# Kernel tuning notes

Hardware: AMD Instinct MI355X
Metric: run time of the kernel (lower is better)

Reference implementation:

```python
import jax, jax.numpy as jnp
import numpy as np


def _maxpool2(t):
    # 2x2x2 max pool, stride 2. t: [B, C, D, H, W]
    B, C, D, H, W = t.shape
    return t.reshape(B, C, D // 2, 2, H // 2, 2, W // 2, 2).max(axis=(3, 5, 7))


def setup_inputs() -> dict:
    key = jax.random.key(0)
    ks = jax.random.split(key, 5)
    ch = 64
    B, D, H, W = 2, 32, 32, 32
    x = jax.random.normal(ks[0], (B, ch, D, H, W), dtype=jnp.float32)
    # 1x1x1 conv weights (out_ch, in_ch), Kaiming-ish scale
    w_theta = jax.random.normal(ks[1], (ch // 8, ch), dtype=jnp.float32) / np.sqrt(ch)
    w_phi = jax.random.normal(ks[2], (ch // 8, ch), dtype=jnp.float32) / np.sqrt(ch)
    w_g = jax.random.normal(ks[3], (ch // 2, ch), dtype=jnp.float32) / np.sqrt(ch)
    w_o = jax.random.normal(ks[4], (ch, ch // 2), dtype=jnp.float32) / np.sqrt(ch // 2)
    gamma = jnp.ones((), dtype=jnp.float32)  # original inits at 0; 1 gives nontrivial output
    return {"x": x, "w_theta": w_theta, "w_phi": w_phi, "w_g": w_g, "w_o": w_o, "gamma": gamma}


def reference(x, w_theta, w_phi, w_g, w_o, gamma):
    B, C, D, H, W = x.shape
    N = D * H * W
    M = N // 8
    xf = x.reshape(B, C, N)  # [B, C, N]
    # 1x1x1 convs = channel matmuls
    theta = jnp.einsum('oc,bcn->bon', w_theta, xf)                     # [B, C//8, N]
    phi = _maxpool2(jnp.einsum('oc,bcn->bon', w_phi, xf).reshape(B, C // 8, D, H, W)).reshape(B, C // 8, M)
    g = _maxpool2(jnp.einsum('oc,bcn->bon', w_g, xf).reshape(B, C // 2, D, H, W)).reshape(B, C // 2, M)
    # unscaled attention: softmax over keys (M)
    beta = jax.nn.softmax(jnp.einsum('bcn,bcm->bnm', theta, phi), axis=-1)  # [B, N, M]
    o = jnp.einsum('bcm,bnm->bcn', g, beta)                                 # [B, C//2, N]
    out = gamma * jnp.einsum('oc,bcn->bon', w_o, o).reshape(B, C, D, H, W) + x
    return out
```

## Files before the change

### kernel.cpp

```cpp
#include <hip/hip_runtime.h>
#include <cstdint>
#include <cstddef>

typedef __attribute__((ext_vector_type(4))) short short4v;
typedef __attribute__((ext_vector_type(4))) float float4v;

#define C_IN  64
#define NB    2
#define NPTS  32768
#define MPTS  4096
#define LOG2E 1.44269504088896340736f
#define KT    64
#define NTILE (MPTS / KT)
#define QTILES (NPTS / 32)

__device__ __forceinline__ unsigned short f2bf_rne(float f) {
  unsigned int u = __builtin_bit_cast(unsigned int, f);
  u += 0x7fffu + ((u >> 16) & 1u);
  return (unsigned short)(u >> 16);
}

__device__ __forceinline__ short4v pack_bf16_trunc(float a0, float a1, float a2, float a3) {
  unsigned int u0 = __builtin_amdgcn_perm(__builtin_bit_cast(unsigned int, a1),
                                          __builtin_bit_cast(unsigned int, a0), 0x07060302u);
  unsigned int u1 = __builtin_amdgcn_perm(__builtin_bit_cast(unsigned int, a3),
                                          __builtin_bit_cast(unsigned int, a2), 0x07060302u);
  union { unsigned int u[2]; short4v s; } r;
  r.u[0] = u0; r.u[1] = u1;
  return r.s;
}

__device__ __forceinline__ short4v pack_bf16_rne(float a0, float a1, float a2, float a3) {
  short4v s;
  s[0] = (short)f2bf_rne(a0); s[1] = (short)f2bf_rne(a1);
  s[2] = (short)f2bf_rne(a2); s[3] = (short)f2bf_rne(a3);
  return s;
}

__device__ __forceinline__ void gl_lds16(const unsigned short* g, unsigned short* l) {
  __builtin_amdgcn_global_load_lds(
      (const __attribute__((address_space(1))) void*)g,
      (__attribute__((address_space(3))) void*)l, 16, 0, 0);
}


__device__ void pool_body(int idx, const float* __restrict__ x,
                          const float* __restrict__ w_phi,
                          const float* __restrict__ w_g,
                          unsigned short* __restrict__ phi_f,
                          unsigned short* __restrict__ g_f) {
  int cg = idx >> 13;
  int bm = idx & 8191;
  int b = bm >> 12, m = bm & 4095;
  int md = m >> 8, mh = (m >> 4) & 15, mw = m & 15;
  const float* xb = x + (size_t)b * C_IN * NPTS
                  + ((md * 2) * 1024 + (mh * 2) * 32 + (mw * 2));
  const float* wbase = (cg == 0) ? w_phi : (w_g + (cg - 1) * 8 * C_IN);

  float acc[8][8];
#pragma unroll
  for (int o = 0; o < 8; ++o)
#pragma unroll
    for (int p = 0; p < 8; ++p) acc[o][p] = 0.f;

#pragma unroll 4
  for (int cc = 0; cc < C_IN; ++cc) {
    const float* xp = xb + (size_t)cc * NPTS;
    float2 p01 = *(const float2*)(xp + 0);
    float2 p23 = *(const float2*)(xp + 32);
    float2 p45 = *(const float2*)(xp + 1024);
    float2 p67 = *(const float2*)(xp + 1056);
#pragma unroll
    for (int o = 0; o < 8; ++o) {
      float wv = wbase[o * C_IN + cc];
      acc[o][0] = fmaf(wv, p01.x, acc[o][0]);
      acc[o][1] = fmaf(wv, p01.y, acc[o][1]);
      acc[o][2] = fmaf(wv, p23.x, acc[o][2]);
      acc[o][3] = fmaf(wv, p23.y, acc[o][3]);
      acc[o][4] = fmaf(wv, p45.x, acc[o][4]);
      acc[o][5] = fmaf(wv, p45.y, acc[o][5]);
      acc[o][6] = fmaf(wv, p67.x, acc[o][6]);
      acc[o][7] = fmaf(wv, p67.y, acc[o][7]);
    }
  }
  float mx[8];
#pragma unroll
  for (int o = 0; o < 8; ++o) {
    mx[o] = fmaxf(fmaxf(fmaxf(acc[o][0], acc[o][1]), fmaxf(acc[o][2], acc[o][3])),
                  fmaxf(fmaxf(acc[o][4], acc[o][5]), fmaxf(acc[o][6], acc[o][7])));
  }
  int kt16 = m >> 4, kr = m & 15;
  if (cg == 0) {
    size_t fb = ((size_t)b * 256 + kt16) * 256;
#pragma unroll
    for (int g2 = 0; g2 < 2; ++g2) {
      unsigned int u0 = (unsigned int)f2bf_rne(mx[g2 * 4 + 0] * LOG2E)
                      | ((unsigned int)f2bf_rne(mx[g2 * 4 + 1] * LOG2E) << 16);
      unsigned int u1 = (unsigned int)f2bf_rne(mx[g2 * 4 + 2] * LOG2E)
                      | ((unsigned int)f2bf_rne(mx[g2 * 4 + 3] * LOG2E) << 16);
      *(uint2*)&phi_f[fb + (g2 * 16 + kr) * 4] = make_uint2(u0, u1);
    }
#pragma unroll
    for (int g2 = 2; g2 < 4; ++g2) {
      *(uint2*)&phi_f[fb + (g2 * 16 + kr) * 4] = make_uint2(0u, 0u);
    }
  } else {
    int gc0 = (cg - 1) * 8;
#pragma unroll
    for (int o = 0; o < 8; ++o) {
      int c = gc0 + o;
      int half = c >> 4, c15 = c & 15;
      size_t base = (((size_t)b * 256 + kt16) * 2 + half) * 256;
      g_f[base + ((kr >> 2) * 16 + c15) * 4 + (kr & 3)] = f2bf_rne(mx[o]);
    }
  }
}

__device__ void theta_body(int idx, const float* __restrict__ x,
                           const float* __restrict__ w_theta,
                           unsigned short* __restrict__ theta_pad) {
  int b = idx >> 15, n = idx & 32767;
  const float* xb = x + (size_t)b * C_IN * NPTS + n;
  float t[8];
#pragma unroll
  for (int o = 0; o < 8; ++o) t[o] = 0.f;
#pragma unroll 4
  for (int cc = 0; cc < C_IN; ++cc) {
    float xv = xb[(size_t)cc * NPTS];
#pragma unroll
    for (int o = 0; o < 8; ++o) t[o] = fmaf(w_theta[o * C_IN + cc], xv, t[o]);
  }
  unsigned int w0 = (unsigned int)f2bf_rne(t[0]) | ((unsigned int)f2bf_rne(t[1]) << 16);
  unsigned int w1 = (unsigned int)f2bf_rne(t[2]) | ((unsigned int)f2bf_rne(t[3]) << 16);
  unsigned int w2 = (unsigned int)f2bf_rne(t[4]) | ((unsigned int)f2bf_rne(t[5]) << 16);
  unsigned int w3 = (unsigned int)f2bf_rne(t[6]) | ((unsigned int)f2bf_rne(t[7]) << 16);
  uint4* dst = (uint4*)(theta_pad + ((size_t)idx << 4));
  dst[0] = make_uint4(w0, w1, w2, w3);
  dst[1] = make_uint4(0u, 0u, 0u, 0u);
}

__global__ __launch_bounds__(256) void prep_fused(
    const float* __restrict__ x, const float* __restrict__ w_theta,
    const float* __restrict__ w_phi, const float* __restrict__ w_g,
    unsigned short* __restrict__ theta_pad,
    unsigned short* __restrict__ phi_f,
    unsigned short* __restrict__ g_f) {
  int gb = blockIdx.x;
  if (gb < 160) {
    pool_body(gb * 256 + threadIdx.x, x, w_phi, w_g, phi_f, g_f);
  } else {
    theta_body((gb - 160) * 256 + threadIdx.x, x, w_theta, theta_pad);
  }
}

template <int KS>
__global__ __launch_bounds__(256) void attn_split(
    const unsigned short* __restrict__ theta_pad,
    const unsigned short* __restrict__ phi_f,
    const unsigned short* __restrict__ g_f,
    float4v* __restrict__ opart,
    float* __restrict__ lbuf) {
  __shared__ unsigned short s_phi[2][KT * 16];
  __shared__ unsigned short s_g[2][(KT / 16) * 512];

  int tid = threadIdx.x;
  int wid = tid >> 6, lane = tid & 63;
  int l4 = lane >> 4, col = lane & 15;
  int b = blockIdx.y / KS;
  int ks = blockIdx.y & (KS - 1);
  int qb = blockIdx.x * 128 + wid * 32;
  int t0 = ks * (NTILE / KS);
  int t1 = t0 + NTILE / KS;

  const unsigned short* tb = theta_pad + ((size_t)(b * NPTS + qb) << 4) + l4 * 4;
  short4v bt0 = *(const short4v*)(tb + (col << 4));
  short4v bt1 = *(const short4v*)(tb + ((16 + col) << 4));

  const unsigned short* phib = phi_f + (size_t)b * 256 * 256;
  const unsigned short* gb   = g_f + (size_t)b * 256 * 512;

  float4v acc00 = {0.f, 0.f, 0.f, 0.f}, acc01 = acc00, acc10 = acc00, acc11 = acc00;
  float lsum0 = 0.f, lsum1 = 0.f;

  gl_lds16(gb + (size_t)t0 * 2048 + wid * 512 + lane * 8, &s_g[0][wid * 512]);
  if (wid < 2)
    gl_lds16(phib + (size_t)t0 * 1024 + wid * 512 + lane * 8, &s_phi[0][wid * 512]);
  __syncthreads();

#pragma unroll 1
  for (int t = t0; t < t1; ++t) {
    int cur = t & 1;
    if (t + 1 < t1) {
      gl_lds16(gb + (size_t)(t + 1) * 2048 + wid * 512 + lane * 8,
               &s_g[cur ^ 1][wid * 512]);
      if (wid < 2)
        gl_lds16(phib + (size_t)(t + 1) * 1024 + wid * 512 + lane * 8,
                 &s_phi[cur ^ 1][wid * 512]);
    }

#pragma unroll
    for (int st = 0; st < 4; ++st) {
      short4v pf = *(const short4v*)&s_phi[cur][st * 256 + lane * 4];
      short4v g0 = *(const short4v*)&s_g[cur][st * 512 + lane * 4];
      short4v g1 = *(const short4v*)&s_g[cur][st * 512 + 256 + lane * 4];

      float4v zero4 = {0.f, 0.f, 0.f, 0.f};
      float4v s0 = __builtin_amdgcn_mfma_f32_16x16x16bf16_1k(pf, bt0, zero4, 0, 0, 0);
      float4v s1 = __builtin_amdgcn_mfma_f32_16x16x16bf16_1k(pf, bt1, zero4, 0, 0, 0);

      float p00 = __builtin_amdgcn_exp2f(s0[0]);
      float p01 = __builtin_amdgcn_exp2f(s0[1]);
      float p02 = __builtin_amdgcn_exp2f(s0[2]);
      float p03 = __builtin_amdgcn_exp2f(s0[3]);
      float p10 = __builtin_amdgcn_exp2f(s1[0]);
      float p11 = __builtin_amdgcn_exp2f(s1[1]);
      float p12 = __builtin_amdgcn_exp2f(s1[2]);
      float p13 = __builtin_amdgcn_exp2f(s1[3]);
      lsum0 += (p00 + p01) + (p02 + p03);
      lsum1 += (p10 + p11) + (p12 + p13);
      short4v pb0 = pack_bf16_trunc(p00, p01, p02, p03);
      short4v pb1 = pack_bf16_trunc(p10, p11, p12, p13);

      acc00 = __builtin_amdgcn_mfma_f32_16x16x16bf16_1k(g0, pb0, acc00, 0, 0, 0);
      acc01 = __builtin_amdgcn_mfma_f32_16x16x16bf16_1k(g0, pb1, acc01, 0, 0, 0);
      acc10 = __builtin_amdgcn_mfma_f32_16x16x16bf16_1k(g1, pb0, acc10, 0, 0, 0);
      acc11 = __builtin_amdgcn_mfma_f32_16x16x16bf16_1k(g1, pb1, acc11, 0, 0, 0);
    }
    __syncthreads();
  }

  lsum0 += __shfl_xor(lsum0, 16, 64);
  lsum0 += __shfl_xor(lsum0, 32, 64);
  lsum1 += __shfl_xor(lsum1, 16, 64);
  lsum1 += __shfl_xor(lsum1, 32, 64);

  int qt = blockIdx.x * 4 + wid;
  size_t obase = (((size_t)(b * KS + ks) * QTILES + qt) * 4) * 64 + lane;
  opart[obase + 0 * 64] = acc00;
  opart[obase + 1 * 64] = acc01;
  opart[obase + 2 * 64] = acc10;
  opart[obase + 3 * 64] = acc11;
  if (lane < 32) {
    lbuf[((size_t)(b * KS + ks) * QTILES + qt) * 32 + lane] =
        (lane < 16) ? lsum0 : lsum1;
  }
}

template <int KS>
__global__ __launch_bounds__(256) void attn_combine(
    const float* __restrict__ x, const float* __restrict__ w_o,
    const float* __restrict__ gamma_p,
    const float4v* __restrict__ opart,
    const float* __restrict__ lbuf,
    float* __restrict__ out) {
  int tid = threadIdx.x;
  int wid = tid >> 6, lane = tid & 63;
  int l4 = lane >> 4, col = lane & 15;
  int b = blockIdx.y;
  int qt = blockIdx.x * 4 + wid;
  int qb = qt * 32;

  float gamma = gamma_p[0];

  short4v wo[4][2];
#pragma unroll
  for (int cot = 0; cot < 4; ++cot)
#pragma unroll
    for (int ksw = 0; ksw < 2; ++ksw) {
      const float* wp = w_o + (cot * 16 + col) * 32 + ksw * 16 + l4 * 4;
      wo[cot][ksw] = pack_bf16_rne(wp[0] * gamma, wp[1] * gamma,
                                   wp[2] * gamma, wp[3] * gamma);
    }

  float4v a0 = {0.f, 0.f, 0.f, 0.f}, a1 = a0, a2 = a0, a3 = a0;
  float ls0 = 0.f, ls1 = 0.f;
#pragma unroll
  for (int ks = 0; ks < KS; ++ks) {
    size_t ob = (((size_t)(b * KS + ks) * QTILES + qt) * 4) * 64 + lane;
    a0 += opart[ob + 0 * 64];
    a1 += opart[ob + 1 * 64];
    a2 += opart[ob + 2 * 64];
    a3 += opart[ob + 3 * 64];
    const float* lb = lbuf + ((size_t)(b * KS + ks) * QTILES + qt) * 32;
    ls0 += lb[col];
    ls1 += lb[col + 16];
  }
  float li0 = 1.0f / ls0;
  float li1 = 1.0f / ls1;

  short4v onb00 = pack_bf16_rne(a0[0] * li0, a0[1] * li0, a0[2] * li0, a0[3] * li0);
  short4v onb01 = pack_bf16_rne(a1[0] * li1, a1[1] * li1, a1[2] * li1, a1[3] * li1);
  short4v onb10 = pack_bf16_rne(a2[0] * li0, a2[1] * li0, a2[2] * li0, a2[3] * li0);
  short4v onb11 = pack_bf16_rne(a3[0] * li1, a3[1] * li1, a3[2] * li1, a3[3] * li1);

  float4v zero4 = {0.f, 0.f, 0.f, 0.f};
#pragma unroll
  for (int cot = 0; cot < 4; ++cot) {
#pragma unroll
    for (int nt = 0; nt < 2; ++nt) {
      short4v bfrag0 = nt ? onb01 : onb00;
      short4v bfrag1 = nt ? onb11 : onb10;
      float4v d = __builtin_amdgcn_mfma_f32_16x16x16bf16_1k(wo[cot][0], bfrag0, zero4, 0, 0, 0);
      d = __builtin_amdgcn_mfma_f32_16x16x16bf16_1k(wo[cot][1], bfrag1, d, 0, 0, 0);
      int n = qb + nt * 16 + col;
      size_t base = (size_t)(b * C_IN + cot * 16 + l4 * 4) * NPTS + n;
      const float* xp = x + base;
      float* op = out + base;
#pragma unroll
      for (int e = 0; e < 4; ++e) {
        op[(size_t)e * NPTS] = d[e] + xp[(size_t)e * NPTS];
      }
    }
  }
}

__global__ __launch_bounds__(256) void attn_mfma(
    const float* __restrict__ x, const float* __restrict__ w_o,
    const float* __restrict__ gamma_p,
    const unsigned short* __restrict__ theta_pad,
    const unsigned short* __restrict__ phi_f,
    const unsigned short* __restrict__ g_f,
    float* __restrict__ out) {
  __shared__ unsigned short s_phi[2][KT * 16];
  __shared__ unsigned short s_g[2][(KT / 16) * 512];

  int tid = threadIdx.x;
  int wid = tid >> 6, lane = tid & 63;
  int l4 = lane >> 4, col = lane & 15;
  int b = blockIdx.y;
  int qb = blockIdx.x * 128 + wid * 32;

  float gamma = gamma_p[0];

  const unsigned short* tb = theta_pad + ((size_t)(b * NPTS + qb) << 4) + l4 * 4;
  short4v bt0 = *(const short4v*)(tb + (col << 4));
  short4v bt1 = *(const short4v*)(tb + ((16 + col) << 4));

  short4v wo[4][2];
#pragma unroll
  for (int cot = 0; cot < 4; ++cot)
#pragma unroll
    for (int ksw = 0; ksw < 2; ++ksw) {
      const float* wp = w_o + (cot * 16 + col) * 32 + ksw * 16 + l4 * 4;
      wo[cot][ksw] = pack_bf16_rne(wp[0] * gamma, wp[1] * gamma,
                                   wp[2] * gamma, wp[3] * gamma);
    }

  const unsigned short* phib = phi_f + (size_t)b * 256 * 256;
  const unsigned short* gb   = g_f + (size_t)b * 256 * 512;

  float4v acc00 = {0.f, 0.f, 0.f, 0.f}, acc01 = acc00, acc10 = acc00, acc11 = acc00;
  float lsum0 = 0.f, lsum1 = 0.f;

  gl_lds16(gb + 0 * 2048 + wid * 512 + lane * 8, &s_g[0][wid * 512]);
  if (wid < 2)
    gl_lds16(phib + 0 * 1024 + wid * 512 + lane * 8, &s_phi[0][wid * 512]);
  __syncthreads();

#pragma unroll 1
  for (int t = 0; t < NTILE; ++t) {
    int cur = t & 1;
    if (t + 1 < NTILE) {
      gl_lds16(gb + (size_t)(t + 1) * 2048 + wid * 512 + lane * 8,
               &s_g[cur ^ 1][wid * 512]);
      if (wid < 2)
        gl_lds16(phib + (size_t)(t + 1) * 1024 + wid * 512 + lane * 8,
                 &s_phi[cur ^ 1][wid * 512]);
    }
#pragma unroll
    for (int st = 0; st < 4; ++st) {
      short4v pf = *(const short4v*)&s_phi[cur][st * 256 + lane * 4];
      short4v g0 = *(const short4v*)&s_g[cur][st * 512 + lane * 4];
      short4v g1 = *(const short4v*)&s_g[cur][st * 512 + 256 + lane * 4];

      float4v zero4 = {0.f, 0.f, 0.f, 0.f};
      float4v s0 = __builtin_amdgcn_mfma_f32_16x16x16bf16_1k(pf, bt0, zero4, 0, 0, 0);
      float4v s1 = __builtin_amdgcn_mfma_f32_16x16x16bf16_1k(pf, bt1, zero4, 0, 0, 0);

      float p00 = __builtin_amdgcn_exp2f(s0[0]);
      float p01 = __builtin_amdgcn_exp2f(s0[1]);
      float p02 = __builtin_amdgcn_exp2f(s0[2]);
      float p03 = __builtin_amdgcn_exp2f(s0[3]);
      float p10 = __builtin_amdgcn_exp2f(s1[0]);
      float p11 = __builtin_amdgcn_exp2f(s1[1]);
      float p12 = __builtin_amdgcn_exp2f(s1[2]);
      float p13 = __builtin_amdgcn_exp2f(s1[3]);
      lsum0 += (p00 + p01) + (p02 + p03);
      lsum1 += (p10 + p11) + (p12 + p13);
      short4v pb0 = pack_bf16_trunc(p00, p01, p02, p03);
      short4v pb1 = pack_bf16_trunc(p10, p11, p12, p13);

      acc00 = __builtin_amdgcn_mfma_f32_16x16x16bf16_1k(g0, pb0, acc00, 0, 0, 0);
      acc01 = __builtin_amdgcn_mfma_f32_16x16x16bf16_1k(g0, pb1, acc01, 0, 0, 0);
      acc10 = __builtin_amdgcn_mfma_f32_16x16x16bf16_1k(g1, pb0, acc10, 0, 0, 0);
      acc11 = __builtin_amdgcn_mfma_f32_16x16x16bf16_1k(g1, pb1, acc11, 0, 0, 0);
    }
    __syncthreads();
  }

  lsum0 += __shfl_xor(lsum0, 16, 64);
  lsum0 += __shfl_xor(lsum0, 32, 64);
  lsum1 += __shfl_xor(lsum1, 16, 64);
  lsum1 += __shfl_xor(lsum1, 32, 64);
  float li0 = 1.0f / lsum0;
  float li1 = 1.0f / lsum1;

  short4v onb00 = pack_bf16_rne(acc00[0] * li0, acc00[1] * li0, acc00[2] * li0, acc00[3] * li0);
  short4v onb01 = pack_bf16_rne(acc01[0] * li1, acc01[1] * li1, acc01[2] * li1, acc01[3] * li1);
  short4v onb10 = pack_bf16_rne(acc10[0] * li0, acc10[1] * li0, acc10[2] * li0, acc10[3] * li0);
  short4v onb11 = pack_bf16_rne(acc11[0] * li1, acc11[1] * li1, acc11[2] * li1, acc11[3] * li1);

  float4v zero4 = {0.f, 0.f, 0.f, 0.f};
#pragma unroll
  for (int cot = 0; cot < 4; ++cot) {
#pragma unroll
    for (int nt = 0; nt < 2; ++nt) {
      short4v bfrag0 = nt ? onb01 : onb00;
      short4v bfrag1 = nt ? onb11 : onb10;
      float4v d = __builtin_amdgcn_mfma_f32_16x16x16bf16_1k(wo[cot][0], bfrag0, zero4, 0, 0, 0);
      d = __builtin_amdgcn_mfma_f32_16x16x16bf16_1k(wo[cot][1], bfrag1, d, 0, 0, 0);
      int n = qb + nt * 16 + col;
      size_t base = (size_t)(b * C_IN + cot * 16 + l4 * 4) * NPTS + n;
      const float* xp = x + base;
      float* op = out + base;
#pragma unroll
      for (int e = 0; e < 4; ++e) {
        op[(size_t)e * NPTS] = d[e] + xp[(size_t)e * NPTS];
      }
    }
  }
}

extern "C" void kernel_launch(void* const* d_in, const int* in_sizes, int n_in,
                              void* d_out, int out_size, void* d_ws, size_t ws_size,
                              hipStream_t stream) {
  const float* x       = (const float*)d_in[0];
  const float* w_theta = (const float*)d_in[1];
  const float* w_phi   = (const float*)d_in[2];
  const float* w_g     = (const float*)d_in[3];
  const float* w_o     = (const float*)d_in[4];
  const float* gamma   = (const float*)d_in[5];
  float* out = (float*)d_out;

  char* ws = (char*)d_ws;
  unsigned short* theta_pad = (unsigned short*)ws;  ws += (size_t)NB * NPTS * 16 * 2;
  unsigned short* phi_f     = (unsigned short*)ws;  ws += (size_t)NB * 256 * 256 * 2;
  unsigned short* g_f       = (unsigned short*)ws;  ws += (size_t)NB * 256 * 512 * 2;
  size_t base_need = (size_t)(ws - (char*)d_ws);
  float4v* opart = (float4v*)ws;
  size_t opart4 = (size_t)NB * 4 * QTILES * 4 * 64 * sizeof(float4v);
  size_t opart2 = (size_t)NB * 2 * QTILES * 4 * 64 * sizeof(float4v);
  size_t lbuf4  = (size_t)NB * 4 * QTILES * 32 * sizeof(float);
  size_t lbuf2  = (size_t)NB * 2 * QTILES * 32 * sizeof(float);
  size_t need4 = base_need + opart4 + lbuf4;
  size_t need2 = base_need + opart2 + lbuf2;

  prep_fused<<<dim3(416), dim3(256), 0, stream>>>(
      x, w_theta, w_phi, w_g, theta_pad, phi_f, g_f);

  if (ws_size >= need4) {
    float* lbuf = (float*)((char*)opart + opart4);
    attn_split<4><<<dim3(NPTS / 128, NB * 4), dim3(256), 0, stream>>>(
        theta_pad, phi_f, g_f, opart, lbuf);
    attn_combine<4><<<dim3(NPTS / 128, NB), dim3(256), 0, stream>>>(
        x, w_o, gamma, opart, lbuf, out);
  } else if (ws_size >= need2) {
    float* lbuf = (float*)((char*)opart + opart2);
    attn_split<2><<<dim3(NPTS / 128, NB * 2), dim3(256), 0, stream>>>(
        theta_pad, phi_f, g_f, opart, lbuf);
    attn_combine<2><<<dim3(NPTS / 128, NB), dim3(256), 0, stream>>>(
        x, w_o, gamma, opart, lbuf, out);
  } else if (ws_size >= base_need) {
    attn_mfma<<<dim3(NPTS / 128, NB), dim3(256), 0, stream>>>(
        x, w_o, gamma, theta_pad, phi_f, g_f, out);
  }
}
```

Baseline: 96.85 us.

## Read K/V fragments directly from global memory and restructure pooled projection

The attention split kernel stops staging phi/g tiles in LDS through double-buffered global_load_lds and barriers. Each wave now reads its MFMA fragments straight from global memory, relying on L2 because every block reuses the same keys. The split factor drops from 4 to 2. The pooled projection now uses one thread per pre-pool voxel computing all 40 output channels, with the 2x2x2 max done by lane shuffles instead of channel-group threads. This removes LDS traffic and synchronization but exposes the loop to global load latency and halves key-split parallelism.

```diff
diff --git a/kernel.cpp b/kernel.cpp
--- a/kernel.cpp
+++ b/kernel.cpp
@@ -49,69 +49,56 @@
                           const float* __restrict__ w_g,
                           unsigned short* __restrict__ phi_f,
                           unsigned short* __restrict__ g_f) {
-  int cg = idx >> 13;
-  int bm = idx & 8191;
-  int b = bm >> 12, m = bm & 4095;
+  int b = idx >> 15;
+  int rem = idx & 32767;
+  int m = rem >> 3, pos = rem & 7;
   int md = m >> 8, mh = (m >> 4) & 15, mw = m & 15;
-  const float* xb = x + (size_t)b * C_IN * NPTS
-                  + ((md * 2) * 1024 + (mh * 2) * 32 + (mw * 2));
-  const float* wbase = (cg == 0) ? w_phi : (w_g + (cg - 1) * 8 * C_IN);
-
-  float acc[8][8];
-#pragma unroll
-  for (int o = 0; o < 8; ++o)
-#pragma unroll
-    for (int p = 0; p < 8; ++p) acc[o][p] = 0.f;
+  int dd = pos >> 2, hh = (pos >> 1) & 1, ww = pos & 1;
+  int n = (md * 2 + dd) * 1024 + (mh * 2 + hh) * 32 + (mw * 2 + ww);
+  const float* xb = x + (size_t)b * C_IN * NPTS + n;
+
+  float acc[40];
+#pragma unroll
+  for (int o = 0; o < 40; ++o) acc[o] = 0.f;
 
 #pragma unroll 4
   for (int cc = 0; cc < C_IN; ++cc) {
-    const float* xp = xb + (size_t)cc * NPTS;
-    float2 p01 = *(const float2*)(xp + 0);
-    float2 p23 = *(const float2*)(xp + 32);
-    float2 p45 = *(const float2*)(xp + 1024);
-    float2 p67 = *(const float2*)(xp + 1056);
-#pragma unroll
-    for (int o = 0; o < 8; ++o) {
-      float wv = wbase[o * C_IN + cc];
-      acc[o][0] = fmaf(wv, p01.x, acc[o][0]);
-      acc[o][1] = fmaf(wv, p01.y, acc[o][1]);
-      acc[o][2] = fmaf(wv, p23.x, acc[o][2]);
-      acc[o][3] = fmaf(wv, p23.y, acc[o][3]);
-      acc[o][4] = fmaf(wv, p45.x, acc[o][4]);
-      acc[o][5] = fmaf(wv, p45.y, acc[o][5]);
-      acc[o][6] = fmaf(wv, p67.x, acc[o][6]);
-      acc[o][7] = fmaf(wv, p67.y, acc[o][7]);
-    }
-  }
-  float mx[8];
-#pragma unroll
-  for (int o = 0; o < 8; ++o) {
-    mx[o] = fmaxf(fmaxf(fmaxf(acc[o][0], acc[o][1]), fmaxf(acc[o][2], acc[o][3])),
-                  fmaxf(fmaxf(acc[o][4], acc[o][5]), fmaxf(acc[o][6], acc[o][7])));
-  }
-  int kt16 = m >> 4, kr = m & 15;
-  if (cg == 0) {
+    float xv = xb[(size_t)cc * NPTS];
+#pragma unroll
+    for (int o = 0; o < 8; ++o)  acc[o] = fmaf(w_phi[o * C_IN + cc], xv, acc[o]);
+#pragma unroll
+    for (int o = 0; o < 32; ++o) acc[8 + o] = fmaf(w_g[o * C_IN + cc], xv, acc[8 + o]);
+  }
+
+#pragma unroll
+  for (int o = 0; o < 40; ++o) {
+    float v = acc[o];
+    v = fmaxf(v, __shfl_xor(v, 1, 64));
+    v = fmaxf(v, __shfl_xor(v, 2, 64));
+    v = fmaxf(v, __shfl_xor(v, 4, 64));
+    acc[o] = v;
+  }
+
+  if (pos == 0) {
+    int kt16 = m >> 4, kr = m & 15;
     size_t fb = ((size_t)b * 256 + kt16) * 256;
 #pragma unroll
     for (int g2 = 0; g2 < 2; ++g2) {
-      unsigned int u0 = (unsigned int)f2bf_rne(mx[g2 * 4 + 0] * LOG2E)
-                      | ((unsigned int)f2bf_rne(mx[g2 * 4 + 1] * LOG2E) << 16);
-      unsigned int u1 = (unsigned int)f2bf_rne(mx[g2 * 4 + 2] * LOG2E)
-                      | ((unsigned int)f2bf_rne(mx[g2 * 4 + 3] * LOG2E) << 16);
+      unsigned int u0 = (unsigned int)f2bf_rne(acc[g2 * 4 + 0] * LOG2E)
+                      | ((unsigned int)f2bf_rne(acc[g2 * 4 + 1] * LOG2E) << 16);
+      unsigned int u1 = (unsigned int)f2bf_rne(acc[g2 * 4 + 2] * LOG2E)
+                      | ((unsigned int)f2bf_rne(acc[g2 * 4 + 3] * LOG2E) << 16);
       *(uint2*)&phi_f[fb + (g2 * 16 + kr) * 4] = make_uint2(u0, u1);
     }
 #pragma unroll
     for (int g2 = 2; g2 < 4; ++g2) {
       *(uint2*)&phi_f[fb + (g2 * 16 + kr) * 4] = make_uint2(0u, 0u);
     }
-  } else {
-    int gc0 = (cg - 1) * 8;
-#pragma unroll
-    for (int o = 0; o < 8; ++o) {
-      int c = gc0 + o;
-      int half = c >> 4, c15 = c & 15;
+#pragma unroll
+    for (int o = 0; o < 32; ++o) {
+      int half = o >> 4, c15 = o & 15;
       size_t base = (((size_t)b * 256 + kt16) * 2 + half) * 256;
-      g_f[base + ((kr >> 2) * 16 + c15) * 4 + (kr & 3)] = f2bf_rne(mx[o]);
+      g_f[base + ((kr >> 2) * 16 + c15) * 4 + (kr & 3)] = f2bf_rne(acc[8 + o]);
     }
   }
 }
@@ -146,87 +133,66 @@
     unsigned short* __restrict__ phi_f,
     unsigned short* __restrict__ g_f) {
   int gb = blockIdx.x;
-  if (gb < 160) {
+  if (gb < 256) {
     pool_body(gb * 256 + threadIdx.x, x, w_phi, w_g, phi_f, g_f);
   } else {
-    theta_body((gb - 160) * 256 + threadIdx.x, x, w_theta, theta_pad);
+    theta_body((gb - 256) * 256 + threadIdx.x, x, w_theta, theta_pad);
   }
 }
 
 template <int KS>
-__global__ __launch_bounds__(256) void attn_split(
+__global__ __launch_bounds__(256) void attn_split_nl(
     const unsigned short* __restrict__ theta_pad,
     const unsigned short* __restrict__ phi_f,
     const unsigned short* __restrict__ g_f,
     float4v* __restrict__ opart,
     float* __restrict__ lbuf) {
-  __shared__ unsigned short s_phi[2][KT * 16];
-  __shared__ unsigned short s_g[2][(KT / 16) * 512];
-
   int tid = threadIdx.x;
   int wid = tid >> 6, lane = tid & 63;
   int l4 = lane >> 4, col = lane & 15;
   int b = blockIdx.y / KS;
-  int ks = blockIdx.y & (KS - 1);
+  int ks = blockIdx.y % KS;
   int qb = blockIdx.x * 128 + wid * 32;
-  int t0 = ks * (NTILE / KS);
-  int t1 = t0 + NTILE / KS;
 
   const unsigned short* tb = theta_pad + ((size_t)(b * NPTS + qb) << 4) + l4 * 4;
   short4v bt0 = *(const short4v*)(tb + (col << 4));
   short4v bt1 = *(const short4v*)(tb + ((16 + col) << 4));
 
-  const unsigned short* phib = phi_f + (size_t)b * 256 * 256;
-  const unsigned short* gb   = g_f + (size_t)b * 256 * 512;
+  const int FPB = 256 / KS;
+  int f0 = ks * FPB;
+  const unsigned short* pp = phi_f + (size_t)b * 65536 + (size_t)f0 * 256 + lane * 4;
+  const unsigned short* gp = g_f + (size_t)b * 131072 + (size_t)f0 * 512 + lane * 4;
 
   float4v acc00 = {0.f, 0.f, 0.f, 0.f}, acc01 = acc00, acc10 = acc00, acc11 = acc00;
   float lsum0 = 0.f, lsum1 = 0.f;
 
-  gl_lds16(gb + (size_t)t0 * 2048 + wid * 512 + lane * 8, &s_g[0][wid * 512]);
-  if (wid < 2)
-    gl_lds16(phib + (size_t)t0 * 1024 + wid * 512 + lane * 8, &s_phi[0][wid * 512]);
-  __syncthreads();
-
-#pragma unroll 1
-  for (int t = t0; t < t1; ++t) {
-    int cur = t & 1;
-    if (t + 1 < t1) {
-      gl_lds16(gb + (size_t)(t + 1) * 2048 + wid * 512 + lane * 8,
-               &s_g[cur ^ 1][wid * 512]);
-      if (wid < 2)
-        gl_lds16(phib + (size_t)(t + 1) * 1024 + wid * 512 + lane * 8,
-                 &s_phi[cur ^ 1][wid * 512]);
-    }
-
-#pragma unroll
-    for (int st = 0; st < 4; ++st) {
-      short4v pf = *(const short4v*)&s_phi[cur][st * 256 + lane * 4];
-      short4v g0 = *(const short4v*)&s_g[cur][st * 512 + lane * 4];
-      short4v g1 = *(const short4v*)&s_g[cur][st * 512 + 256 + lane * 4];
-
-      float4v zero4 = {0.f, 0.f, 0.f, 0.f};
-      float4v s0 = __builtin_amdgcn_mfma_f32_16x16x16bf16_1k(pf, bt0, zero4, 0, 0, 0);
-      float4v s1 = __builtin_amdgcn_mfma_f32_16x16x16bf16_1k(pf, bt1, zero4, 0, 0, 0);
-
-      float p00 = __builtin_amdgcn_exp2f(s0[0]);
-      float p01 = __builtin_amdgcn_exp2f(s0[1]);
-      float p02 = __builtin_amdgcn_exp2f(s0[2]);
-      float p03 = __builtin_amdgcn_exp2f(s0[3]);
-      float p10 = __builtin_amdgcn_exp2f(s1[0]);
-      float p11 = __builtin_amdgcn_exp2f(s1[1]);
-      float p12 = __builtin_amdgcn_exp2f(s1[2]);
-      float p13 = __builtin_amdgcn_exp2f(s1[3]);
-      lsum0 += (p00 + p01) + (p02 + p03);
-      lsum1 += (p10 + p11) + (p12 + p13);
-      short4v pb0 = pack_bf16_trunc(p00, p01, p02, p03);
-      short4v pb1 = pack_bf16_trunc(p10, p11, p12, p13);
-
-      acc00 = __builtin_amdgcn_mfma_f32_16x16x16bf16_1k(g0, pb0, acc00, 0, 0, 0);
-      acc01 = __builtin_amdgcn_mfma_f32_16x16x16bf16_1k(g0, pb1, acc01, 0, 0, 0);
-      acc10 = __builtin_amdgcn_mfma_f32_16x16x16bf16_1k(g1, pb0, acc10, 0, 0, 0);
-      acc11 = __builtin_amdgcn_mfma_f32_16x16x16bf16_1k(g1, pb1, acc11, 0, 0, 0);
-    }
-    __syncthreads();
+#pragma unroll 4
+  for (int f = 0; f < FPB; ++f) {
+    short4v pf = *(const short4v*)(pp + (size_t)f * 256);
+    short4v g0 = *(const short4v*)(gp + (size_t)f * 512);
+    short4v g1 = *(const short4v*)(gp + (size_t)f * 512 + 256);
+
+    float4v zero4 = {0.f, 0.f, 0.f, 0.f};
+    float4v s0 = __builtin_amdgcn_mfma_f32_16x16x16bf16_1k(pf, bt0, zero4, 0, 0, 0);
+    float4v s1 = __builtin_amdgcn_mfma_f32_16x16x16bf16_1k(pf, bt1, zero4, 0, 0, 0);
+
+    float p00 = __builtin_amdgcn_exp2f(s0[0]);
+    float p01 = __builtin_amdgcn_exp2f(s0[1]);
+    float p02 = __builtin_amdgcn_exp2f(s0[2]);
+    float p03 = __builtin_amdgcn_exp2f(s0[3]);
+    float p10 = __builtin_amdgcn_exp2f(s1[0]);
+    float p11 = __builtin_amdgcn_exp2f(s1[1]);
+    float p12 = __builtin_amdgcn_exp2f(s1[2]);
+    float p13 = __builtin_amdgcn_exp2f(s1[3]);
+    lsum0 += (p00 + p01) + (p02 + p03);
+    lsum1 += (p10 + p11) + (p12 + p13);
+    short4v pb0 = pack_bf16_trunc(p00, p01, p02, p03);
+    short4v pb1 = pack_bf16_trunc(p10, p11, p12, p13);
+
+    acc00 = __builtin_amdgcn_mfma_f32_16x16x16bf16_1k(g0, pb0, acc00, 0, 0, 0);
+    acc01 = __builtin_amdgcn_mfma_f32_16x16x16bf16_1k(g0, pb1, acc01, 0, 0, 0);
+    acc10 = __builtin_amdgcn_mfma_f32_16x16x16bf16_1k(g1, pb0, acc10, 0, 0, 0);
+    acc11 = __builtin_amdgcn_mfma_f32_16x16x16bf16_1k(g1, pb1, acc11, 0, 0, 0);
   }
 
   lsum0 += __shfl_xor(lsum0, 16, 64);
@@ -448,25 +414,16 @@
   unsigned short* g_f       = (unsigned short*)ws;  ws += (size_t)NB * 256 * 512 * 2;
   size_t base_need = (size_t)(ws - (char*)d_ws);
   float4v* opart = (float4v*)ws;
-  size_t opart4 = (size_t)NB * 4 * QTILES * 4 * 64 * sizeof(float4v);
   size_t opart2 = (size_t)NB * 2 * QTILES * 4 * 64 * sizeof(float4v);
-  size_t lbuf4  = (size_t)NB * 4 * QTILES * 32 * sizeof(float);
   size_t lbuf2  = (size_t)NB * 2 * QTILES * 32 * sizeof(float);
-  size_t need4 = base_need + opart4 + lbuf4;
   size_t need2 = base_need + opart2 + lbuf2;
 
-  prep_fused<<<dim3(416), dim3(256), 0, stream>>>(
+  prep_fused<<<dim3(512), dim3(256), 0, stream>>>(
       x, w_theta, w_phi, w_g, theta_pad, phi_f, g_f);
 
-  if (ws_size >= need4) {
-    float* lbuf = (float*)((char*)opart + opart4);
-    attn_split<4><<<dim3(NPTS / 128, NB * 4), dim3(256), 0, stream>>>(
-        theta_pad, phi_f, g_f, opart, lbuf);
-    attn_combine<4><<<dim3(NPTS / 128, NB), dim3(256), 0, stream>>>(
-        x, w_o, gamma, opart, lbuf, out);
-  } else if (ws_size >= need2) {
+  if (ws_size >= need2) {
     float* lbuf = (float*)((char*)opart + opart2);
-    attn_split<2><<<dim3(NPTS / 128, NB * 2), dim3(256), 0, stream>>>(
+    attn_split_nl<2><<<dim3(NPTS / 128, NB * 2), dim3(256), 0, stream>>>(
         theta_pad, phi_f, g_f, opart, lbuf);
     attn_combine<2><<<dim3(NPTS / 128, NB), dim3(256), 0, stream>>>(
         x, w_o, gamma, opart, lbuf, out);
```

Result: no change. 98.20 us (+1.4%).

## Process 64 queries per wave in split attention to reuse key/value LDS tiles

Applied to the files above, without the earlier changes.

The split attention kernel now gives each wave 64 query columns instead of 32, so every phi and g fragment read from LDS feeds four score MFMAs and eight PV MFMAs instead of two and four. The grid halves, and the partial-output and row-sum layouts move to 64-query tiles, with the combine kernel indexing into them accordingly. The goal is to halve LDS traffic and the global tile loads per query, along with the barrier and loop overhead. In exchange each wave holds more registers (eight accumulators and four theta fragments), which is why launch bounds now request 4 blocks, and there are half as many blocks to fill the GPU.

```diff
diff --git a/kernel.cpp b/kernel.cpp
--- a/kernel.cpp
+++ b/kernel.cpp
@@ -12,7 +12,7 @@
 #define LOG2E 1.44269504088896340736f
 #define KT    64
 #define NTILE (MPTS / KT)
-#define QTILES (NPTS / 32)
+#define QT64  (NPTS / 64)
 
 __device__ __forceinline__ unsigned short f2bf_rne(float f) {
   unsigned int u = __builtin_bit_cast(unsigned int, f);
@@ -99,10 +99,7 @@
       unsigned int u1 = (unsigned int)f2bf_rne(mx[g2 * 4 + 2] * LOG2E)
                       | ((unsigned int)f2bf_rne(mx[g2 * 4 + 3] * LOG2E) << 16);
       *(uint2*)&phi_f[fb + (g2 * 16 + kr) * 4] = make_uint2(u0, u1);
-    }
-#pragma unroll
-    for (int g2 = 2; g2 < 4; ++g2) {
-      *(uint2*)&phi_f[fb + (g2 * 16 + kr) * 4] = make_uint2(0u, 0u);
+      *(uint2*)&phi_f[fb + ((g2 + 2) * 16 + kr) * 4] = make_uint2(0u, 0u);
     }
   } else {
     int gc0 = (cg - 1) * 8;
@@ -154,7 +151,7 @@
 }
 
 template <int KS>
-__global__ __launch_bounds__(256) void attn_split(
+__global__ __launch_bounds__(256, 4) void attn_split64(
     const unsigned short* __restrict__ theta_pad,
     const unsigned short* __restrict__ phi_f,
     const unsigned short* __restrict__ g_f,
@@ -167,20 +164,27 @@
   int wid = tid >> 6, lane = tid & 63;
   int l4 = lane >> 4, col = lane & 15;
   int b = blockIdx.y / KS;
-  int ks = blockIdx.y & (KS - 1);
-  int qb = blockIdx.x * 128 + wid * 32;
+  int ks = blockIdx.y % KS;
+  int qb = blockIdx.x * 256 + wid * 64;
+  int qt64 = blockIdx.x * 4 + wid;
   int t0 = ks * (NTILE / KS);
   int t1 = t0 + NTILE / KS;
 
   const unsigned short* tb = theta_pad + ((size_t)(b * NPTS + qb) << 4) + l4 * 4;
-  short4v bt0 = *(const short4v*)(tb + (col << 4));
-  short4v bt1 = *(const short4v*)(tb + ((16 + col) << 4));
-
-  const unsigned short* phib = phi_f + (size_t)b * 256 * 256;
-  const unsigned short* gb   = g_f + (size_t)b * 256 * 512;
-
-  float4v acc00 = {0.f, 0.f, 0.f, 0.f}, acc01 = acc00, acc10 = acc00, acc11 = acc00;
-  float lsum0 = 0.f, lsum1 = 0.f;
+  short4v bt0 = *(const short4v*)(tb + ((0 * 16 + col) << 4));
+  short4v bt1 = *(const short4v*)(tb + ((1 * 16 + col) << 4));
+  short4v bt2 = *(const short4v*)(tb + ((2 * 16 + col) << 4));
+  short4v bt3 = *(const short4v*)(tb + ((3 * 16 + col) << 4));
+
+  const unsigned short* phib = phi_f + (size_t)b * 65536;
+  const unsigned short* gb   = g_f + (size_t)b * 131072;
+
+  float4v acc[2][4];
+#pragma unroll
+  for (int h = 0; h < 2; ++h)
+#pragma unroll
+    for (int j = 0; j < 4; ++j) acc[h][j] = (float4v){0.f, 0.f, 0.f, 0.f};
+  float lsum0 = 0.f, lsum1 = 0.f, lsum2 = 0.f, lsum3 = 0.f;
 
   gl_lds16(gb + (size_t)t0 * 2048 + wid * 512 + lane * 8, &s_g[0][wid * 512]);
   if (wid < 2)
@@ -198,6 +202,199 @@
                  &s_phi[cur ^ 1][wid * 512]);
     }
 
+#pragma unroll
+    for (int st = 0; st < 4; ++st) {
+      short4v pf = *(const short4v*)&s_phi[cur][st * 256 + lane * 4];
+      short4v g0 = *(const short4v*)&s_g[cur][st * 512 + lane * 4];
+      short4v g1 = *(const short4v*)&s_g[cur][st * 512 + 256 + lane * 4];
+
+      float4v zero4 = {0.f, 0.f, 0.f, 0.f};
+      float4v s0 = __builtin_amdgcn_mfma_f32_16x16x16bf16_1k(pf, bt0, zero4, 0, 0, 0);
+      float4v s1 = __builtin_amdgcn_mfma_f32_16x16x16bf16_1k(pf, bt1, zero4, 0, 0, 0);
+      float4v s2 = __builtin_amdgcn_mfma_f32_16x16x16bf16_1k(pf, bt2, zero4, 0, 0, 0);
+      float4v s3 = __builtin_amdgcn_mfma_f32_16x16x16bf16_1k(pf, bt3, zero4, 0, 0, 0);
+
+      float p00 = __builtin_amdgcn_exp2f(s0[0]);
+      float p01 = __builtin_amdgcn_exp2f(s0[1]);
+      float p02 = __builtin_amdgcn_exp2f(s0[2]);
+      float p03 = __builtin_amdgcn_exp2f(s0[3]);
+      float p10 = __builtin_amdgcn_exp2f(s1[0]);
+      float p11 = __builtin_amdgcn_exp2f(s1[1]);
+      float p12 = __builtin_amdgcn_exp2f(s1[2]);
+      float p13 = __builtin_amdgcn_exp2f(s1[3]);
+      float p20 = __builtin_amdgcn_exp2f(s2[0]);
+      float p21 = __builtin_amdgcn_exp2f(s2[1]);
+      float p22 = __builtin_amdgcn_exp2f(s2[2]);
+      float p23 = __builtin_amdgcn_exp2f(s2[3]);
+      float p30 = __builtin_amdgcn_exp2f(s3[0]);
+      float p31 = __builtin_amdgcn_exp2f(s3[1]);
+      float p32 = __builtin_amdgcn_exp2f(s3[2]);
+      float p33 = __builtin_amdgcn_exp2f(s3[3]);
+      lsum0 += (p00 + p01) + (p02 + p03);
+      lsum1 += (p10 + p11) + (p12 + p13);
+      lsum2 += (p20 + p21) + (p22 + p23);
+      lsum3 += (p30 + p31) + (p32 + p33);
+      short4v pb0 = pack_bf16_trunc(p00, p01, p02, p03);
+      short4v pb1 = pack_bf16_trunc(p10, p11, p12, p13);
+      short4v pb2 = pack_bf16_trunc(p20, p21, p22, p23);
+      short4v pb3 = pack_bf16_trunc(p30, p31, p32, p33);
+
+      acc[0][0] = __builtin_amdgcn_mfma_f32_16x16x16bf16_1k(g0, pb0, acc[0][0], 0, 0, 0);
+      acc[0][1] = __builtin_amdgcn_mfma_f32_16x16x16bf16_1k(g0, pb1, acc[0][1], 0, 0, 0);
+      acc[0][2] = __builtin_amdgcn_mfma_f32_16x16x16bf16_1k(g0, pb2, acc[0][2], 0, 0, 0);
+      acc[0][3] = __builtin_amdgcn_mfma_f32_16x16x16bf16_1k(g0, pb3, acc[0][3], 0, 0, 0);
+      acc[1][0] = __builtin_amdgcn_mfma_f32_16x16x16bf16_1k(g1, pb0, acc[1][0], 0, 0, 0);
+      acc[1][1] = __builtin_amdgcn_mfma_f32_16x16x16bf16_1k(g1, pb1, acc[1][1], 0, 0, 0);
+      acc[1][2] = __builtin_amdgcn_mfma_f32_16x16x16bf16_1k(g1, pb2, acc[1][2], 0, 0, 0);
+      acc[1][3] = __builtin_amdgcn_mfma_f32_16x16x16bf16_1k(g1, pb3, acc[1][3], 0, 0, 0);
+    }
+    __syncthreads();
+  }
+
+  lsum0 += __shfl_xor(lsum0, 16, 64);
+  lsum0 += __shfl_xor(lsum0, 32, 64);
+  lsum1 += __shfl_xor(lsum1, 16, 64);
+  lsum1 += __shfl_xor(lsum1, 32, 64);
+  lsum2 += __shfl_xor(lsum2, 16, 64);
+  lsum2 += __shfl_xor(lsum2, 32, 64);
+  lsum3 += __shfl_xor(lsum3, 16, 64);
+  lsum3 += __shfl_xor(lsum3, 32, 64);
+
+  size_t rowb = (size_t)(b * KS + ks) * QT64 + qt64;
+  float myl = (l4 == 0) ? lsum0 : (l4 == 1) ? lsum1 : (l4 == 2) ? lsum2 : lsum3;
+  lbuf[rowb * 64 + lane] = myl;
+
+  size_t obase = rowb * 8 * 64 + lane;
+#pragma unroll
+  for (int h = 0; h < 2; ++h)
+#pragma unroll
+    for (int j = 0; j < 4; ++j)
+      opart[obase + (size_t)(h * 4 + j) * 64] = acc[h][j];
+}
+
+template <int KS>
+__global__ __launch_bounds__(256) void attn_combine(
+    const float* __restrict__ x, const float* __restrict__ w_o,
+    const float* __restrict__ gamma_p,
+    const float4v* __restrict__ opart,
+    const float* __restrict__ lbuf,
+    float* __restrict__ out) {
+  int tid = threadIdx.x;
+  int wid = tid >> 6, lane = tid & 63;
+  int l4 = lane >> 4, col = lane & 15;
+  int b = blockIdx.y;
+  int qt32 = blockIdx.x * 4 + wid;
+  int qb = qt32 * 32;
+  int qt64 = qt32 >> 1, hf = qt32 & 1;
+
+  float gamma = gamma_p[0];
+
+  short4v wo[4][2];
+#pragma unroll
+  for (int cot = 0; cot < 4; ++cot)
+#pragma unroll
+    for (int ksw = 0; ksw < 2; ++ksw) {
+      const float* wp = w_o + (cot * 16 + col) * 32 + ksw * 16 + l4 * 4;
+      wo[cot][ksw] = pack_bf16_rne(wp[0] * gamma, wp[1] * gamma,
+                                   wp[2] * gamma, wp[3] * gamma);
+    }
+
+  float4v a0 = {0.f, 0.f, 0.f, 0.f}, a1 = a0, a2 = a0, a3 = a0;
+  float ls0 = 0.f, ls1 = 0.f;
+#pragma unroll
+  for (int ks = 0; ks < KS; ++ks) {
+    size_t rowb = (size_t)(b * KS + ks) * QT64 + qt64;
+    size_t ob = (rowb * 8 + hf * 2) * 64 + lane;
+    a0 += opart[ob + 0 * 64];
+    a1 += opart[ob + 1 * 64];
+    a2 += opart[ob + 4 * 64];
+    a3 += opart[ob + 5 * 64];
+    const float* lb = lbuf + rowb * 64 + hf * 32;
+    ls0 += lb[col];
+    ls1 += lb[col + 16];
+  }
+  float li0 = 1.0f / ls0;
+  float li1 = 1.0f / ls1;
+
+  short4v onb00 = pack_bf16_rne(a0[0] * li0, a0[1] * li0, a0[2] * li0, a0[3] * li0);
+  short4v onb01 = pack_bf16_rne(a1[0] * li1, a1[1] * li1, a1[2] * li1, a1[3] * li1);
+  short4v onb10 = pack_bf16_rne(a2[0] * li0, a2[1] * li0, a2[2] * li0, a2[3] * li0);
+  short4v onb11 = pack_bf16_rne(a3[0] * li1, a3[1] * li1, a3[2] * li1, a3[3] * li1);
+
+  float4v zero4 = {0.f, 0.f, 0.f, 0.f};
+#pragma unroll
+  for (int cot = 0; cot < 4; ++cot) {
+#pragma unroll
+    for (int nt = 0; nt < 2; ++nt) {
+      short4v bfrag0 = nt ? onb01 : onb00;
+      short4v bfrag1 = nt ? onb11 : onb10;
+      float4v d = __builtin_amdgcn_mfma_f32_16x16x16bf16_1k(wo[cot][0], bfrag0, zero4, 0, 0, 0);
+      d = __builtin_amdgcn_mfma_f32_16x16x16bf16_1k(wo[cot][1], bfrag1, d, 0, 0, 0);
+      int n = qb + nt * 16 + col;
+      size_t base = (size_t)(b * C_IN + cot * 16 + l4 * 4) * NPTS + n;
+      const float* xp = x + base;
+      float* op = out + base;
+#pragma unroll
+      for (int e = 0; e < 4; ++e) {
+        op[(size_t)e * NPTS] = d[e] + xp[(size_t)e * NPTS];
+      }
+    }
+  }
+}
+
+__global__ __launch_bounds__(256) void attn_mfma(
+    const float* __restrict__ x, const float* __restrict__ w_o,
+    const float* __restrict__ gamma_p,
+    const unsigned short* __restrict__ theta_pad,
+    const unsigned short* __restrict__ phi_f,
+    const unsigned short* __restrict__ g_f,
+    float* __restrict__ out) {
+  __shared__ unsigned short s_phi[2][KT * 16];
+  __shared__ unsigned short s_g[2][(KT / 16) * 512];
+
+  int tid = threadIdx.x;
+  int wid = tid >> 6, lane = tid & 63;
+  int l4 = lane >> 4, col = lane & 15;
+  int b = blockIdx.y;
+  int qb = blockIdx.x * 128 + wid * 32;
+
+  float gamma = gamma_p[0];
+
+  const unsigned short* tb = theta_pad + ((size_t)(b * NPTS + qb) << 4) + l4 * 4;
+  short4v bt0 = *(const short4v*)(tb + (col << 4));
+  short4v bt1 = *(const short4v*)(tb + ((16 + col) << 4));
+
+  short4v wo[4][2];
+#pragma unroll
+  for (int cot = 0; cot < 4; ++cot)
+#pragma unroll
+    for (int ksw = 0; ksw < 2; ++ksw) {
+      const float* wp = w_o + (cot * 16 + col) * 32 + ksw * 16 + l4 * 4;
+      wo[cot][ksw] = pack_bf16_rne(wp[0] * gamma, wp[1] * gamma,
+                                   wp[2] * gamma, wp[3] * gamma);
+    }
+
+  const unsigned short* phib = phi_f + (size_t)b * 256 * 256;
+  const unsigned short* gb   = g_f + (size_t)b * 256 * 512;
+
+  float4v acc00 = {0.f, 0.f, 0.f, 0.f}, acc01 = acc00, acc10 = acc00, acc11 = acc00;
+  float lsum0 = 0.f, lsum1 = 0.f;
+
+  gl_lds16(gb + 0 * 2048 + wid * 512 + lane * 8, &s_g[0][wid * 512]);
+  if (wid < 2)
+    gl_lds16(phib + 0 * 1024 + wid * 512 + lane * 8, &s_phi[0][wid * 512]);
+  __syncthreads();
+
+#pragma unroll 1
+  for (int t = 0; t < NTILE; ++t) {
+    int cur = t & 1;
+    if (t + 1 < NTILE) {
+      gl_lds16(gb + (size_t)(t + 1) * 2048 + wid * 512 + lane * 8,
+               &s_g[cur ^ 1][wid * 512]);
+      if (wid < 2)
+        gl_lds16(phib + (size_t)(t + 1) * 1024 + wid * 512 + lane * 8,
+                 &s_phi[cur ^ 1][wid * 512]);
+    }
 #pragma unroll
     for (int st = 0; st < 4; ++st) {
       short4v pf = *(const short4v*)&s_phi[cur][st * 256 + lane * 4];
@@ -233,175 +430,6 @@
   lsum0 += __shfl_xor(lsum0, 32, 64);
   lsum1 += __shfl_xor(lsum1, 16, 64);
   lsum1 += __shfl_xor(lsum1, 32, 64);
-
-  int qt = blockIdx.x * 4 + wid;
-  size_t obase = (((size_t)(b * KS + ks) * QTILES + qt) * 4) * 64 + lane;
-  opart[obase + 0 * 64] = acc00;
-  opart[obase + 1 * 64] = acc01;
-  opart[obase + 2 * 64] = acc10;
-  opart[obase + 3 * 64] = acc11;
-  if (lane < 32) {
-    lbuf[((size_t)(b * KS + ks) * QTILES + qt) * 32 + lane] =
-        (lane < 16) ? lsum0 : lsum1;
-  }
-}
-
-template <int KS>
-__global__ __launch_bounds__(256) void attn_combine(
-    const float* __restrict__ x, const float* __restrict__ w_o,
-    const float* __restrict__ gamma_p,
-    const float4v* __restrict__ opart,
-    const float* __restrict__ lbuf,
-    float* __restrict__ out) {
-  int tid = threadIdx.x;
-  int wid = tid >> 6, lane = tid & 63;
-  int l4 = lane >> 4, col = lane & 15;
-  int b = blockIdx.y;
-  int qt = blockIdx.x * 4 + wid;
-  int qb = qt * 32;
-
-  float gamma = gamma_p[0];
-
-  short4v wo[4][2];
-#pragma unroll
-  for (int cot = 0; cot < 4; ++cot)
-#pragma unroll
-    for (int ksw = 0; ksw < 2; ++ksw) {
-      const float* wp = w_o + (cot * 16 + col) * 32 + ksw * 16 + l4 * 4;
-      wo[cot][ksw] = pack_bf16_rne(wp[0] * gamma, wp[1] * gamma,
-                                   wp[2] * gamma, wp[3] * gamma);
-    }
-
-  float4v a0 = {0.f, 0.f, 0.f, 0.f}, a1 = a0, a2 = a0, a3 = a0;
-  float ls0 = 0.f, ls1 = 0.f;
-#pragma unroll
-  for (int ks = 0; ks < KS; ++ks) {
-    size_t ob = (((size_t)(b * KS + ks) * QTILES + qt) * 4) * 64 + lane;
-    a0 += opart[ob + 0 * 64];
-    a1 += opart[ob + 1 * 64];
-    a2 += opart[ob + 2 * 64];
-    a3 += opart[ob + 3 * 64];
-    const float* lb = lbuf + ((size_t)(b * KS + ks) * QTILES + qt) * 32;
-    ls0 += lb[col];
-    ls1 += lb[col + 16];
-  }
-  float li0 = 1.0f / ls0;
-  float li1 = 1.0f / ls1;
-
-  short4v onb00 = pack_bf16_rne(a0[0] * li0, a0[1] * li0, a0[2] * li0, a0[3] * li0);
-  short4v onb01 = pack_bf16_rne(a1[0] * li1, a1[1] * li1, a1[2] * li1, a1[3] * li1);
-  short4v onb10 = pack_bf16_rne(a2[0] * li0, a2[1] * li0, a2[2] * li0, a2[3] * li0);
-  short4v onb11 = pack_bf16_rne(a3[0] * li1, a3[1] * li1, a3[2] * li1, a3[3] * li1);
-
-  float4v zero4 = {0.f, 0.f, 0.f, 0.f};
-#pragma unroll
-  for (int cot = 0; cot < 4; ++cot) {
-#pragma unroll
-    for (int nt = 0; nt < 2; ++nt) {
-      short4v bfrag0 = nt ? onb01 : onb00;
-      short4v bfrag1 = nt ? onb11 : onb10;
-      float4v d = __builtin_amdgcn_mfma_f32_16x16x16bf16_1k(wo[cot][0], bfrag0, zero4, 0, 0, 0);
-      d = __builtin_amdgcn_mfma_f32_16x16x16bf16_1k(wo[cot][1], bfrag1, d, 0, 0, 0);
-      int n = qb + nt * 16 + col;
-      size_t base = (size_t)(b * C_IN + cot * 16 + l4 * 4) * NPTS + n;
-      const float* xp = x + base;
-      float* op = out + base;
-#pragma unroll
-      for (int e = 0; e < 4; ++e) {
-        op[(size_t)e * NPTS] = d[e] + xp[(size_t)e * NPTS];
-      }
-    }
-  }
-}
-
-__global__ __launch_bounds__(256) void attn_mfma(
-    const float* __restrict__ x, const float* __restrict__ w_o,
-    const float* __restrict__ gamma_p,
-    const unsigned short* __restrict__ theta_pad,
-    const unsigned short* __restrict__ phi_f,
-    const unsigned short* __restrict__ g_f,
-    float* __restrict__ out) {
-  __shared__ unsigned short s_phi[2][KT * 16];
-  __shared__ unsigned short s_g[2][(KT / 16) * 512];
-
-  int tid = threadIdx.x;
-  int wid = tid >> 6, lane = tid & 63;
-  int l4 = lane >> 4, col = lane & 15;
-  int b = blockIdx.y;
-  int qb = blockIdx.x * 128 + wid * 32;
-
-  float gamma = gamma_p[0];
-
-  const unsigned short* tb = theta_pad + ((size_t)(b * NPTS + qb) << 4) + l4 * 4;
-  short4v bt0 = *(const short4v*)(tb + (col << 4));
-  short4v bt1 = *(const short4v*)(tb + ((16 + col) << 4));
-
-  short4v wo[4][2];
-#pragma unroll
-  for (int cot = 0; cot < 4; ++cot)
-#pragma unroll
-    for (int ksw = 0; ksw < 2; ++ksw) {
-      const float* wp = w_o + (cot * 16 + col) * 32 + ksw * 16 + l4 * 4;
-      wo[cot][ksw] = pack_bf16_rne(wp[0] * gamma, wp[1] * gamma,
-                                   wp[2] * gamma, wp[3] * gamma);
-    }
-
-  const unsigned short* phib = phi_f + (size_t)b * 256 * 256;
-  const unsigned short* gb   = g_f + (size_t)b * 256 * 512;
-
-  float4v acc00 = {0.f, 0.f, 0.f, 0.f}, acc01 = acc00, acc10 = acc00, acc11 = acc00;
-  float lsum0 = 0.f, lsum1 = 0.f;
-
-  gl_lds16(gb + 0 * 2048 + wid * 512 + lane * 8, &s_g[0][wid * 512]);
-  if (wid < 2)
-    gl_lds16(phib + 0 * 1024 + wid * 512 + lane * 8, &s_phi[0][wid * 512]);
-  __syncthreads();
-
-#pragma unroll 1
-  for (int t = 0; t < NTILE; ++t) {
-    int cur = t & 1;
-    if (t + 1 < NTILE) {
-      gl_lds16(gb + (size_t)(t + 1) * 2048 + wid * 512 + lane * 8,
-               &s_g[cur ^ 1][wid * 512]);
-      if (wid < 2)
-        gl_lds16(phib + (size_t)(t + 1) * 1024 + wid * 512 + lane * 8,
-                 &s_phi[cur ^ 1][wid * 512]);
-    }
-#pragma unroll
-    for (int st = 0; st < 4; ++st) {
-      short4v pf = *(const short4v*)&s_phi[cur][st * 256 + lane * 4];
-      short4v g0 = *(const short4v*)&s_g[cur][st * 512 + lane * 4];
-      short4v g1 = *(const short4v*)&s_g[cur][st * 512 + 256 + lane * 4];
-
-      float4v zero4 = {0.f, 0.f, 0.f, 0.f};
-      float4v s0 = __builtin_amdgcn_mfma_f32_16x16x16bf16_1k(pf, bt0, zero4, 0, 0, 0);
-      float4v s1 = __builtin_amdgcn_mfma_f32_16x16x16bf16_1k(pf, bt1, zero4, 0, 0, 0);
-
-      float p00 = __builtin_amdgcn_exp2f(s0[0]);
-      float p01 = __builtin_amdgcn_exp2f(s0[1]);
-      float p02 = __builtin_amdgcn_exp2f(s0[2]);
-      float p03 = __builtin_amdgcn_exp2f(s0[3]);
-      float p10 = __builtin_amdgcn_exp2f(s1[0]);
-      float p11 = __builtin_amdgcn_exp2f(s1[1]);
-      float p12 = __builtin_amdgcn_exp2f(s1[2]);
-      float p13 = __builtin_amdgcn_exp2f(s1[3]);
-      lsum0 += (p00 + p01) + (p02 + p03);
-      lsum1 += (p10 + p11) + (p12 + p13);
-      short4v pb0 = pack_bf16_trunc(p00, p01, p02, p03);
-      short4v pb1 = pack_bf16_trunc(p10, p11, p12, p13);
-
-      acc00 = __builtin_amdgcn_mfma_f32_16x16x16bf16_1k(g0, pb0, acc00, 0, 0, 0);
-      acc01 = __builtin_amdgcn_mfma_f32_16x16x16bf16_1k(g0, pb1, acc01, 0, 0, 0);
-      acc10 = __builtin_amdgcn_mfma_f32_16x16x16bf16_1k(g1, pb0, acc10, 0, 0, 0);
-      acc11 = __builtin_amdgcn_mfma_f32_16x16x16bf16_1k(g1, pb1, acc11, 0, 0, 0);
-    }
-    __syncthreads();
-  }
-
-  lsum0 += __shfl_xor(lsum0, 16, 64);
-  lsum0 += __shfl_xor(lsum0, 32, 64);
-  lsum1 += __shfl_xor(lsum1, 16, 64);
-  lsum1 += __shfl_xor(lsum1, 32, 64);
   float li0 = 1.0f / lsum0;
   float li1 = 1.0f / lsum1;
 
@@ -443,15 +471,15 @@
   float* out = (float*)d_out;
 
   char* ws = (char*)d_ws;
-  unsigned short* theta_pad = (unsigned short*)ws;  ws += (size_t)NB * NPTS * 16 * 2;
   unsigned short* phi_f     = (unsigned short*)ws;  ws += (size_t)NB * 256 * 256 * 2;
   unsigned short* g_f       = (unsigned short*)ws;  ws += (size_t)NB * 256 * 512 * 2;
+  unsigned short* theta_pad = (unsigned short*)ws;  ws += (size_t)NB * NPTS * 16 * 2;
   size_t base_need = (size_t)(ws - (char*)d_ws);
   float4v* opart = (float4v*)ws;
-  size_t opart4 = (size_t)NB * 4 * QTILES * 4 * 64 * sizeof(float4v);
-  size_t opart2 = (size_t)NB * 2 * QTILES * 4 * 64 * sizeof(float4v);
-  size_t lbuf4  = (size_t)NB * 4 * QTILES * 32 * sizeof(float);
-  size_t lbuf2  = (size_t)NB * 2 * QTILES * 32 * sizeof(float);
+  size_t opart4 = (size_t)NB * 4 * QT64 * 8 * 64 * sizeof(float4v);
+  size_t opart2 = (size_t)NB * 2 * QT64 * 8 * 64 * sizeof(float4v);
+  size_t lbuf4  = (size_t)NB * 4 * QT64 * 64 * sizeof(float);
+  size_t lbuf2  = (size_t)NB * 2 * QT64 * 64 * sizeof(float);
   size_t need4 = base_need + opart4 + lbuf4;
   size_t need2 = base_need + opart2 + lbuf2;
 
@@ -460,13 +488,13 @@
 
   if (ws_size >= need4) {
     float* lbuf = (float*)((char*)opart + opart4);
-    attn_split<4><<<dim3(NPTS / 128, NB * 4), dim3(256), 0, stream>>>(
+    attn_split64<4><<<dim3(NPTS / 256, NB * 4), dim3(256), 0, stream>>>(
         theta_pad, phi_f, g_f, opart, lbuf);
     attn_combine<4><<<dim3(NPTS / 128, NB), dim3(256), 0, stream>>>(
         x, w_o, gamma, opart, lbuf, out);
   } else if (ws_size >= need2) {
     float* lbuf = (float*)((char*)opart + opart2);
-    attn_split<2><<<dim3(NPTS / 128, NB * 2), dim3(256), 0, stream>>>(
+    attn_split64<2><<<dim3(NPTS / 256, NB * 2), dim3(256), 0, stream>>>(
         theta_pad, phi_f, g_f, opart, lbuf);
     attn_combine<2><<<dim3(NPTS / 128, NB), dim3(256), 0, stream>>>(
         x, w_o, gamma, opart, lbuf, out);
```

After: 92.91 us. -4.1%, faster.
